# Kernel optimization log

Measured on AMD Instinct MI355X. Metric: run time of the kernel, lower is better.

## Reference

```python
import math
import jax, jax.numpy as jnp
import numpy as np

D_MODEL = 512
NUM_HEADS = 8
D_TRACK = 64
EPS = 1e-6


def setup_inputs() -> dict:
    key = jax.random.key(0)
    ks = jax.random.split(key, 8)
    B, C, T = 2, 4096, 16
    lecun = lambda k, shp: jax.random.normal(k, shp, jnp.float32) / jnp.sqrt(jnp.float32(shp[0]))
    return {
        "x": jax.random.normal(ks[0], (B, C, D_MODEL), jnp.float32),
        "track_embeddings": jax.random.normal(ks[1], (B, T, C, D_TRACK), jnp.float32),
        "norm_scale": jnp.ones((D_MODEL,), jnp.float32),
        "wq": lecun(ks[2], (D_MODEL, D_MODEL)), "bq": jnp.zeros((D_MODEL,), jnp.float32),
        "wk": lecun(ks[3], (D_TRACK, D_MODEL)), "bk": jnp.zeros((D_MODEL,), jnp.float32),
        "wv": lecun(ks[4], (D_TRACK, D_MODEL)), "bv": jnp.zeros((D_MODEL,), jnp.float32),
        "wo": lecun(ks[5], (D_MODEL, D_MODEL)), "bo": jnp.zeros((D_MODEL,), jnp.float32),
    }


def reference(x, track_embeddings, norm_scale, wq, bq, wk, bk, wv, bv, wo, bo):
    B, C, D = x.shape
    T = track_embeddings.shape[1]
    H = NUM_HEADS
    d_head = D // H
    residual = x
    # RMSNorm
    xn = x * jax.lax.rsqrt(jnp.mean(jnp.square(x), axis=-1, keepdims=True) + EPS) * norm_scale
    Q = (xn @ wq + bq).reshape(B, C, H, d_head)
    track_flat = track_embeddings.transpose(0, 2, 1, 3)  # (B, C, T, d_track)
    K = (track_flat @ wk + bk).reshape(B, C, T, H, d_head)
    V = (track_flat @ wv + bv).reshape(B, C, T, H, d_head)
    scale = 1.0 / math.sqrt(d_head)
    attn_logits = jnp.einsum('bchd,bcthd->bcht', Q, K) * scale
    attn_weights = jax.nn.softmax(attn_logits, axis=-1)
    attn_out = jnp.einsum('bcht,bcthd->bchd', attn_weights, V).reshape(B, C, D)
    return residual + attn_out @ wo + bo
```

## Files before the change

### kernel.cpp

```cpp
#include <hip/hip_runtime.h>
#include <math.h>


#define NTOK 8192

typedef __attribute__((ext_vector_type(8))) short short8;
typedef __attribute__((ext_vector_type(8))) unsigned short ushort8;
typedef __attribute__((ext_vector_type(4))) unsigned short ushort4v;
typedef __attribute__((ext_vector_type(4))) float f32x4;

__device__ __forceinline__ unsigned short f2bf(float f) {
    unsigned int u = __float_as_uint(f);
    unsigned int r = (u + 0x7fffu + ((u >> 16) & 1u)) >> 16;
    return (unsigned short)r;
}
__device__ __forceinline__ float bf2f(unsigned short s) {
    return __uint_as_float(((unsigned int)s) << 16);
}

__device__ __forceinline__ void gl_lds16(const void* g, void* l) {
    __builtin_amdgcn_global_load_lds(
        (const __attribute__((address_space(1))) unsigned int*)g,
        (__attribute__((address_space(3))) unsigned int*)l,
        16, 0, 0);
}


__global__ __launch_bounds__(256) void kprep(
    const float* __restrict__ x, const float* __restrict__ nscale,
    const float* __restrict__ wq, const float* __restrict__ bq,
    const float* __restrict__ wk, const float* __restrict__ wv,
    const float* __restrict__ bv, const float* __restrict__ wo,
    const float* __restrict__ bo,
    unsigned short* __restrict__ wqkT, float* __restrict__ bqk,
    unsigned short* __restrict__ wvoT, float* __restrict__ bvo,
    unsigned short* __restrict__ xnb)
{
    const int bid = blockIdx.x;
    const int t = threadIdx.x;
    if (bid < 64) {
        __shared__ float wkL[64][65];
        __shared__ float wqL[64][65];
        const int h = bid >> 3;
        const int i0 = (bid & 7) * 64;
        #pragma unroll
        for (int i = 0; i < 16; ++i) {
            const int idx = t + i * 256;
            const int d = idx >> 6, e = idx & 63;
            wkL[d][e] = wk[(size_t)d * 512 + h * 64 + e];
            wqL[d][e] = wq[(size_t)(i0 + d) * 512 + h * 64 + e];
        }
        __syncthreads();
        const int d = t & 63, ig = t >> 6;
        float acc[16];
        #pragma unroll
        for (int ii = 0; ii < 16; ++ii) acc[ii] = 0.f;
        for (int e = 0; e < 64; ++e) {
            const float kv = wkL[d][e];
            #pragma unroll
            for (int ii = 0; ii < 16; ++ii)
                acc[ii] += kv * wqL[ig * 16 + ii][e];
        }
        #pragma unroll
        for (int ii = 0; ii < 16; ++ii)
            wqkT[(size_t)(h * 64 + d) * 512 + i0 + ig * 16 + ii] = f2bf(acc[ii]);
        if (((bid & 7) == 0) && ig == 0) {
            float a = 0.f;
            #pragma unroll
            for (int e = 0; e < 64; ++e) a += bq[h * 64 + e] * wkL[d][e];
            bqk[h * 64 + d] = a;
        }
    } else if (bid < 128) {
        __shared__ float wvL[64][65];
        __shared__ float woL[64][65];
        const int b2 = bid - 64;
        const int h = b2 >> 3;
        const int j0 = (b2 & 7) * 64;
        #pragma unroll
        for (int i = 0; i < 16; ++i) {
            const int idx = t + i * 256;
            const int a = idx >> 6, b = idx & 63;
            wvL[a][b] = wv[(size_t)a * 512 + h * 64 + b];
            woL[a][b] = wo[(size_t)(h * 64 + a) * 512 + j0 + b];
        }
        __syncthreads();
        const int jloc = t & 63, dg = t >> 6;
        float acc[16];
        #pragma unroll
        for (int dd = 0; dd < 16; ++dd) acc[dd] = 0.f;
        for (int e = 0; e < 64; ++e) {
            const float b = woL[e][jloc];
            #pragma unroll
            for (int dd = 0; dd < 16; ++dd)
                acc[dd] += wvL[dg * 16 + dd][e] * b;
        }
        #pragma unroll
        for (int dd = 0; dd < 16; ++dd)
            wvoT[(size_t)(j0 + jloc) * 512 + h * 64 + dg * 16 + dd] = f2bf(acc[dd]);
    } else if (bid < 192) {
        const int b3 = bid - 128;
        const int j = b3 * 8 + (t >> 5);
        const int l = t & 31;
        float p = 0.f;
        #pragma unroll 4
        for (int e = l; e < 512; e += 32) p += bv[e] * wo[(size_t)e * 512 + j];
        #pragma unroll
        for (int m = 1; m < 32; m <<= 1) p += __shfl_xor(p, m, 64);
        if (l == 0) bvo[j] = bo[j] + p;
    } else {
        const int row = (bid - 192) * 4 + (t >> 6);
        const int lane = t & 63;
        const float* xr = x + (size_t)row * 512 + lane * 8;
        const float4 v0 = *reinterpret_cast<const float4*>(xr);
        const float4 v1 = *reinterpret_cast<const float4*>(xr + 4);
        float s = v0.x*v0.x + v0.y*v0.y + v0.z*v0.z + v0.w*v0.w
                + v1.x*v1.x + v1.y*v1.y + v1.z*v1.z + v1.w*v1.w;
        #pragma unroll
        for (int m = 1; m < 64; m <<= 1) s += __shfl_xor(s, m, 64);
        const float r = rsqrtf(s * (1.f / 512.f) + 1e-6f);
        const float4 s0 = *reinterpret_cast<const float4*>(nscale + lane * 8);
        const float4 s1 = *reinterpret_cast<const float4*>(nscale + lane * 8 + 4);
        ushort8 o;
        o[0] = f2bf(v0.x * r * s0.x); o[1] = f2bf(v0.y * r * s0.y);
        o[2] = f2bf(v0.z * r * s0.z); o[3] = f2bf(v0.w * r * s0.w);
        o[4] = f2bf(v1.x * r * s1.x); o[5] = f2bf(v1.y * r * s1.y);
        o[6] = f2bf(v1.z * r * s1.z); o[7] = f2bf(v1.w * r * s1.w);
        *reinterpret_cast<ushort8*>(xnb + (size_t)row * 512 + lane * 8) = o;
    }
}


template<int MODE>
__global__ __launch_bounds__(256) void kG(
    const unsigned short* __restrict__ A,
    const unsigned short* __restrict__ Bt,
    const float* __restrict__ bias,
    const float* __restrict__ resid,
    void* __restrict__ outp)
{
    __shared__ __align__(16) unsigned short Asm[2][128 * 64];
    __shared__ __align__(16) unsigned short Bsm[2][64 * 64];
    const int tid = threadIdx.x;
    const int hw = blockIdx.x;
    const int logical = (hw & 7) * 64 + (hw >> 3);
    const int mt = logical >> 3, nt = logical & 7;
    const int tok0 = mt * 128, n0 = nt * 64;
    const int w = tid >> 6, lane = tid & 63;
    const int wr = w >> 1, wc = w & 1;
    const int lrow = lane & 15, lk = lane >> 4;

    float pb[2];
    float rr[2][4][4];
    #pragma unroll
    for (int n = 0; n < 2; ++n) {
        const int ocol = n0 + wc * 32 + n * 16 + lrow;
        pb[n] = bias[ocol];
        if (MODE == 1) {
            #pragma unroll
            for (int m = 0; m < 4; ++m)
                #pragma unroll
                for (int r = 0; r < 4; ++r) {
                    const int orow = tok0 + wr * 64 + m * 16 + lk * 4 + r;
                    rr[n][m][r] = resid[(size_t)orow * 512 + ocol];
                }
        }
    }

    const int srowA[4] = { (tid + 0) >> 3, (tid + 256) >> 3, (tid + 512) >> 3, (tid + 768) >> 3 };
    const int sc8 = tid & 7;

    auto STAGE = [&](int buf, int k0) {
        #pragma unroll
        for (int i = 0; i < 4; ++i) {
            const int f = tid + i * 256;
            const int row = srowA[i];
            const int c8s = sc8 ^ (row & 7);
            gl_lds16(A + (size_t)(tok0 + row) * 512 + k0 + c8s * 8,
                     (char*)&Asm[buf][0] + f * 16);
        }
        #pragma unroll
        for (int i = 0; i < 2; ++i) {
            const int f = tid + i * 256;
            const int row = f >> 3;
            const int c8s = sc8 ^ (row & 7);
            gl_lds16(Bt + (size_t)(n0 + row) * 512 + k0 + c8s * 8,
                     (char*)&Bsm[buf][0] + f * 16);
        }
    };

    f32x4 acc[4][2] = {};
    STAGE(0, 0);
    __syncthreads();
    for (int it = 0; it < 8; ++it) {
        const int cur = it & 1;
        if (it < 7) STAGE(cur ^ 1, (it + 1) * 64);
        #pragma unroll
        for (int kk = 0; kk < 2; ++kk) {
            short8 a[4], b[2];
            #pragma unroll
            for (int m = 0; m < 4; ++m) {
                const int r = wr * 64 + m * 16 + lrow;
                const int byte = (r * 128 + kk * 64 + lk * 16) ^ ((r & 7) << 4);
                a[m] = *reinterpret_cast<const short8*>((const char*)&Asm[cur][0] + byte);
            }
            #pragma unroll
            for (int n = 0; n < 2; ++n) {
                const int r = wc * 32 + n * 16 + lrow;
                const int byte = (r * 128 + kk * 64 + lk * 16) ^ ((r & 7) << 4);
                b[n] = *reinterpret_cast<const short8*>((const char*)&Bsm[cur][0] + byte);
            }
            #pragma unroll
            for (int m = 0; m < 4; ++m)
                #pragma unroll
                for (int n = 0; n < 2; ++n)
                    acc[m][n] = __builtin_amdgcn_mfma_f32_16x16x32_bf16(
                        a[m], b[n], acc[m][n], 0, 0, 0);
        }
        __syncthreads();
    }
    #pragma unroll
    for (int n = 0; n < 2; ++n) {
        const int ocol = n0 + wc * 32 + n * 16 + lrow;
        #pragma unroll
        for (int m = 0; m < 4; ++m) {
            #pragma unroll
            for (int r = 0; r < 4; ++r) {
                const int orow = tok0 + wr * 64 + m * 16 + lk * 4 + r;
                float v = acc[m][n][r] + pb[n];
                if (MODE == 0) {
                    ((unsigned short*)outp)[(size_t)orow * 512 + ocol] = f2bf(v);
                } else {
                    v += rr[n][m][r];
                    ((float*)outp)[(size_t)orow * 512 + ocol] = v;
                }
            }
        }
    }
}


__global__ __launch_bounds__(256) void k3_attn(
    const float* __restrict__ track, const unsigned short* __restrict__ qwb,
    unsigned short* __restrict__ wtfb)
{
    __shared__ __align__(16) float tf[2][16][68];
    __shared__ __align__(16) float qwl[2][8][68];
    __shared__ float lw[2][8][16];
    const int tid = threadIdx.x;
    const int tok = tid >> 7;
    const int t2 = tid & 127;
    const int hw = blockIdx.x;
    const int logical = (hw & 7) * 512 + (hw >> 3);
    const int token = logical * 2 + tok;
    const int b = token >> 12;
    const int c = token & 4095;
    #pragma unroll
    for (int i = 0; i < 2; ++i) {
        const int f = t2 + i * 128;
        const int row = f >> 4, d4 = (f & 15) * 4;
        *reinterpret_cast<float4*>(&tf[tok][row][d4]) =
            *reinterpret_cast<const float4*>(track + ((size_t)(b * 16 + row) * 4096 + c) * 64 + d4);
    }
    if (t2 < 64) {
        const ushort8 q = *reinterpret_cast<const ushort8*>(qwb + (size_t)token * 512 + t2 * 8);
        #pragma unroll
        for (int j = 0; j < 8; ++j) {
            const int idx = t2 * 8 + j;
            qwl[tok][idx >> 6][idx & 63] = bf2f(q[j]);
        }
    }
    __syncthreads();
    {
        const int h = t2 >> 4, tt = t2 & 15;
        float acc = 0.f;
        #pragma unroll
        for (int d16 = 0; d16 < 16; ++d16) {
            const float4 qv = *reinterpret_cast<const float4*>(&qwl[tok][h][d16 * 4]);
            const float4 tv = *reinterpret_cast<const float4*>(&tf[tok][tt][d16 * 4]);
            acc += qv.x * tv.x + qv.y * tv.y + qv.z * tv.z + qv.w * tv.w;
        }
        float lg = acc * 0.125f;
        float mx = lg;
        #pragma unroll
        for (int m = 1; m < 16; m <<= 1) mx = fmaxf(mx, __shfl_xor(mx, m, 64));
        const float ev = __expf(lg - mx);
        float sum = ev;
        #pragma unroll
        for (int m = 1; m < 16; m <<= 1) sum += __shfl_xor(sum, m, 64);
        lw[tok][h][tt] = ev / sum;
    }
    __syncthreads();
    {
        const int h = t2 >> 4;
        const int d0 = (t2 & 15) * 4;
        float o0 = 0.f, o1 = 0.f, o2 = 0.f, o3 = 0.f;
        #pragma unroll
        for (int t = 0; t < 16; ++t) {
            const float wgt = lw[tok][h][t];
            const float4 tv = *reinterpret_cast<const float4*>(&tf[tok][t][d0]);
            o0 += wgt * tv.x; o1 += wgt * tv.y; o2 += wgt * tv.z; o3 += wgt * tv.w;
        }
        ushort4v ov;
        ov[0] = f2bf(o0); ov[1] = f2bf(o1); ov[2] = f2bf(o2); ov[3] = f2bf(o3);
        *reinterpret_cast<ushort4v*>(wtfb + (size_t)token * 512 + t2 * 4) = ov;
    }
}

extern "C" void kernel_launch(void* const* d_in, const int* in_sizes, int n_in,
                              void* d_out, int out_size, void* d_ws, size_t ws_size,
                              hipStream_t stream) {
    const float* x      = (const float*)d_in[0];
    const float* track  = (const float*)d_in[1];
    const float* nscale = (const float*)d_in[2];
    const float* wq     = (const float*)d_in[3];
    const float* bq     = (const float*)d_in[4];
    const float* wk     = (const float*)d_in[5];
    const float* wv     = (const float*)d_in[7];
    const float* bv     = (const float*)d_in[8];
    const float* wo     = (const float*)d_in[9];
    const float* bo     = (const float*)d_in[10];
    float* buf = (float*)d_out;

    char* ws = (char*)d_ws;
    unsigned short* xnb  = (unsigned short*)ws;
    unsigned short* qwb  = (unsigned short*)(ws + 8388608);
    unsigned short* wtfb = (unsigned short*)(ws + 16777216);
    unsigned short* wqkT = (unsigned short*)(ws + 25165824);
    unsigned short* wvoT = (unsigned short*)(ws + 25690112);
    float* bqk = (float*)(ws + 26214400);
    float* bvo = (float*)(ws + 26216448);

    kprep<<<192 + NTOK / 4, 256, 0, stream>>>(x, nscale, wq, bq, wk, wv, bv, wo, bo,
                                              wqkT, bqk, wvoT, bvo, xnb);
    kG<0><<<512, 256, 0, stream>>>(xnb, wqkT, bqk, nullptr, qwb);
    k3_attn<<<NTOK / 2, 256, 0, stream>>>(track, qwb, wtfb);
    kG<1><<<512, 256, 0, stream>>>(wtfb, wvoT, bvo, x, buf);
}
```

Baseline: 51.49 us.

## Prefetch two stages ahead in GEMM and pipeline attention loads via direct-to-LDS

The GEMM main loop now issues tile loads two iterations ahead and uses explicit vmcnt waits plus raw barriers instead of __syncthreads, so global loads overlap more with MFMA work. The attention kernel now handles four tokens per block. It stages track and query rows straight into LDS with global_load_lds, using a swizzled layout, in two phases so the second pair's loads overlap with compute on the first. Softmax weights are passed through lane shuffles instead of an LDS array. This adds reliance on exact vmcnt counts and fewer blocks for the attention launch.

Result: slower. 52.86 us (+2.7%).

```diff
diff --git a/kernel.cpp b/kernel.cpp
--- a/kernel.cpp
+++ b/kernel.cpp
@@ -190,10 +190,13 @@
 
     f32x4 acc[4][2] = {};
     STAGE(0, 0);
-    __syncthreads();
+    STAGE(1, 64);
     for (int it = 0; it < 8; ++it) {
         const int cur = it & 1;
-        if (it < 7) STAGE(cur ^ 1, (it + 1) * 64);
+        if (it < 7) asm volatile("s_waitcnt vmcnt(6)" ::: "memory");
+        else        asm volatile("s_waitcnt vmcnt(0)" ::: "memory");
+        __builtin_amdgcn_s_barrier();
+        __builtin_amdgcn_sched_barrier(0);
         #pragma unroll
         for (int kk = 0; kk < 2; ++kk) {
             short8 a[4], b[2];
@@ -216,7 +219,10 @@
                     acc[m][n] = __builtin_amdgcn_mfma_f32_16x16x32_bf16(
                         a[m], b[n], acc[m][n], 0, 0, 0);
         }
-        __syncthreads();
+        __builtin_amdgcn_sched_barrier(0);
+        __builtin_amdgcn_s_barrier();
+        __builtin_amdgcn_sched_barrier(0);
+        if (it < 6) STAGE(cur, (it + 2) * 64);
     }
     #pragma unroll
     for (int n = 0; n < 2; ++n) {
@@ -243,62 +249,70 @@
     const float* __restrict__ track, const unsigned short* __restrict__ qwb,
     unsigned short* __restrict__ wtfb)
 {
-    __shared__ __align__(16) float tf[2][16][68];
-    __shared__ __align__(16) float qwl[2][8][68];
-    __shared__ float lw[2][8][16];
+    __shared__ __align__(16) char tfL[2][8192];
+    __shared__ __align__(16) char qwL[4096];
     const int tid = threadIdx.x;
+    const int hw = blockIdx.x;
+    const int logical = (hw & 7) * 256 + (hw >> 3);
+    const int tok0 = logical * 4;
+    const int lane = tid & 63;
+
+    {
+        const int jt = tid >> 6, c = tid & 63;
+        gl_lds16(qwb + (size_t)(tok0 + jt) * 512 + c * 8, qwL + tid * 16);
+    }
+    auto stageTF = [&](int p) {
+        #pragma unroll
+        for (int i = 0; i < 2; ++i) {
+            const int f = tid + i * 256;
+            const int j = f >> 8, t = (f >> 4) & 15, ch = f & 15;
+            const int token = tok0 + p * 2 + j;
+            const int b = token >> 12, c = token & 4095;
+            gl_lds16(track + ((size_t)(b * 16 + t) * 4096 + c) * 64 + ((ch ^ (t & 7)) << 2),
+                     tfL[p] + f * 16);
+        }
+    };
+    stageTF(0);
+    stageTF(1);
+
     const int tok = tid >> 7;
     const int t2 = tid & 127;
-    const int hw = blockIdx.x;
-    const int logical = (hw & 7) * 512 + (hw >> 3);
-    const int token = logical * 2 + tok;
-    const int b = token >> 12;
-    const int c = token & 4095;
+    const int h = t2 >> 4, tt = t2 & 15;
     #pragma unroll
-    for (int i = 0; i < 2; ++i) {
-        const int f = t2 + i * 128;
-        const int row = f >> 4, d4 = (f & 15) * 4;
-        *reinterpret_cast<float4*>(&tf[tok][row][d4]) =
-            *reinterpret_cast<const float4*>(track + ((size_t)(b * 16 + row) * 4096 + c) * 64 + d4);
-    }
-    if (t2 < 64) {
-        const ushort8 q = *reinterpret_cast<const ushort8*>(qwb + (size_t)token * 512 + t2 * 8);
-        #pragma unroll
-        for (int j = 0; j < 8; ++j) {
-            const int idx = t2 * 8 + j;
-            qwl[tok][idx >> 6][idx & 63] = bf2f(q[j]);
-        }
-    }
-    __syncthreads();
-    {
-        const int h = t2 >> 4, tt = t2 & 15;
+    for (int p = 0; p < 2; ++p) {
+        if (p == 0) asm volatile("s_waitcnt vmcnt(2)" ::: "memory");
+        else        asm volatile("s_waitcnt vmcnt(0)" ::: "memory");
+        __builtin_amdgcn_s_barrier();
+        __builtin_amdgcn_sched_barrier(0);
+        const char* tb = tfL[p] + tok * 4096;
+        const char* qb = qwL + (p * 2 + tok) * 1024;
+        const int token = tok0 + p * 2 + tok;
         float acc = 0.f;
         #pragma unroll
-        for (int d16 = 0; d16 < 16; ++d16) {
-            const float4 qv = *reinterpret_cast<const float4*>(&qwl[tok][h][d16 * 4]);
-            const float4 tv = *reinterpret_cast<const float4*>(&tf[tok][tt][d16 * 4]);
-            acc += qv.x * tv.x + qv.y * tv.y + qv.z * tv.z + qv.w * tv.w;
+        for (int ch = 0; ch < 16; ++ch) {
+            const ushort4v qv = *reinterpret_cast<const ushort4v*>(qb + h * 128 + ch * 8);
+            const float4 tv = *reinterpret_cast<const float4*>(
+                tb + tt * 256 + ((ch ^ (tt & 7)) << 4));
+            acc += bf2f(qv[0]) * tv.x + bf2f(qv[1]) * tv.y
+                 + bf2f(qv[2]) * tv.z + bf2f(qv[3]) * tv.w;
         }
         float lg = acc * 0.125f;
         float mx = lg;
         #pragma unroll
         for (int m = 1; m < 16; m <<= 1) mx = fmaxf(mx, __shfl_xor(mx, m, 64));
         const float ev = __expf(lg - mx);
-        float sum = ev;
-        #pragma unroll
-        for (int m = 1; m < 16; m <<= 1) sum += __shfl_xor(sum, m, 64);
-        lw[tok][h][tt] = ev / sum;
-    }
-    __syncthreads();
-    {
-        const int h = t2 >> 4;
-        const int d0 = (t2 & 15) * 4;
+        float sm = ev;
+        #pragma unroll
+        for (int m = 1; m < 16; m <<= 1) sm += __shfl_xor(sm, m, 64);
+        const float pw = ev / sm;
+        const int chp = t2 & 15;
         float o0 = 0.f, o1 = 0.f, o2 = 0.f, o3 = 0.f;
         #pragma unroll
         for (int t = 0; t < 16; ++t) {
-            const float wgt = lw[tok][h][t];
-            const float4 tv = *reinterpret_cast<const float4*>(&tf[tok][t][d0]);
-            o0 += wgt * tv.x; o1 += wgt * tv.y; o2 += wgt * tv.z; o3 += wgt * tv.w;
+            const float wt = __shfl(pw, (lane & 48) + t, 64);
+            const float4 tv = *reinterpret_cast<const float4*>(
+                tb + t * 256 + ((chp ^ (t & 7)) << 4));
+            o0 += wt * tv.x; o1 += wt * tv.y; o2 += wt * tv.z; o3 += wt * tv.w;
         }
         ushort4v ov;
         ov[0] = f2bf(o0); ov[1] = f2bf(o1); ov[2] = f2bf(o2); ov[3] = f2bf(o3);
@@ -333,6 +347,6 @@
     kprep<<<192 + NTOK / 4, 256, 0, stream>>>(x, nscale, wq, bq, wk, wv, bv, wo, bo,
                                               wqkT, bqk, wvoT, bvo, xnb);
     kG<0><<<512, 256, 0, stream>>>(xnb, wqkT, bqk, nullptr, qwb);
-    k3_attn<<<NTOK / 2, 256, 0, stream>>>(track, qwb, wtfb);
+    k3_attn<<<NTOK / 4, 256, 0, stream>>>(track, qwb, wtfb);
     kG<1><<<512, 256, 0, stream>>>(wtfb, wvoT, bvo, x, buf);
 }
```
